# Optimization experiments

Measured on AMD Instinct MI355X. Metric: run time of the kernel, lower is better.

The kernel has to match this reference:

```python
import jax, jax.numpy as jnp
import numpy as np

DIM = 512
DEPTH = 4
E = 2 ** DEPTH          # 16 experts
HID = 4 * DIM           # mult = 4
B, S = 8, 4096


def setup_inputs() -> dict:
    key = jax.random.key(0)
    ks = jax.random.split(key, 7)
    sc_in = 1.0 / np.sqrt(DIM)
    sc_hid = 1.0 / np.sqrt(HID)
    return {
        "x": jax.random.normal(ks[0], (B, S, DIM), jnp.float32),
        "Wr": jax.random.normal(ks[1], (E - 1, DIM), jnp.float32) * sc_in,
        "br": jax.random.normal(ks[2], (E - 1,), jnp.float32) * 0.01,
        "W1": jax.random.normal(ks[3], (E, DIM, HID), jnp.float32) * sc_in,
        "b1": jax.random.normal(ks[4], (E, HID), jnp.float32) * 0.01,
        "W2": jax.random.normal(ks[5], (E, HID, DIM), jnp.float32) * sc_hid,
        "b2": jax.random.normal(ks[6], (E, DIM), jnp.float32) * 0.01,
    }


def _fff_forward(x, Wr, br, W1, b1, W2, b2):
    Bb, Ss, D = x.shape
    E_ = W1.shape[0]
    depth = int(np.log2(E_))
    xf = x.reshape(-1, D)                      # [N, D]
    N = xf.shape[0]

    # Hard binary-tree routing (inference path of the torch module).
    leaf = jnp.zeros((N,), jnp.int32)
    for d in range(depth):
        off = 2 ** d - 1
        cnt = 2 ** d
        # logits for all routers at this tree level: [N, cnt]
        logits = xf @ Wr[off:off + cnt].T + br[off:off + cnt]
        sel = jnp.take_along_axis(logits, leaf[:, None], axis=1)[:, 0]
        leaf = leaf * 2 + (sel > 0).astype(jnp.int32)

    onehot = jax.nn.one_hot(leaf, E_, dtype=xf.dtype)  # [N, E]

    # Dense weighted-sum dispatch: scan over the (small, fixed) expert axis,
    # accumulating masked expert outputs. Peak extra memory is one [N, HID]
    # activation at a time.
    def body(acc, params):
        w1, bb1, w2, bb2, m = params            # m: [N]
        h = jax.nn.gelu(xf @ w1 + bb1, approximate=False)  # exact GELU (torch nn.GELU)
        y = h @ w2 + bb2
        return acc + m[:, None] * y, None

    out, _ = jax.lax.scan(body, jnp.zeros_like(xf), (W1, b1, W2, b2, onehot.T))
    return out.reshape(Bb, Ss, D)


def reference(x, Wr, br, W1, b1, W2, b2):
    return _fff_forward(x, Wr, br, W1, b1, W2, b2)
```

## Files before the change

kernel.cpp:

```cpp
#include <hip/hip_runtime.h>
#include <math.h>

#define NTOK   32768
#define DMODEL 512
#define HIDDEN 2048
#define NEXP   16
#define TM     256
#define MAXT   144
#define PADN   (MAXT * TM)
#define CPAD   16

typedef short bf16x8 __attribute__((ext_vector_type(8)));
typedef float f32x4  __attribute__((ext_vector_type(4)));

__device__ __forceinline__ short f2bf(float f) {
  union { float f; unsigned int u; } v; v.f = f;
  unsigned int r = v.u + 0x7FFFu + ((v.u >> 16) & 1u);
  return (short)(r >> 16);
}

__device__ __forceinline__ void gload_lds16(const void* g, void* l) {
  __builtin_amdgcn_global_load_lds(
      (const __attribute__((address_space(1))) void*)g,
      (__attribute__((address_space(3))) void*)l, 16, 0, 0);
}

__device__ __forceinline__ float gelu_f(float v) {
  const float u = v * (0.7978845608f + 0.0356774081f * v * v);
  const float au = fabsf(u);
  const float z = __expf(-2.0f * au);
  float T = (1.0f - z) / (1.0f + z);
  T = copysignf(T, u);
  return 0.5f * v * (1.0f + T);
}

__global__ void init_kernel(int* counts, int* cursors) {
  counts[threadIdx.x] = 0; cursors[threadIdx.x] = 0;
}

__global__ __launch_bounds__(256) void route_kernel(
    const float* __restrict__ x, const float* __restrict__ Wr,
    const float* __restrict__ br, short* __restrict__ xb,
    int* __restrict__ leafArr) {
  const int w = threadIdx.x >> 6, l = threadIdx.x & 63;
  const int tok = blockIdx.x * 4 + w;
  const float4* xr = (const float4*)(x + (size_t)tok * DMODEL);
  float4 a0 = xr[l * 2], a1 = xr[l * 2 + 1];

  union { bf16x8 v; short s[8]; } u;
  u.s[0] = f2bf(a0.x); u.s[1] = f2bf(a0.y); u.s[2] = f2bf(a0.z); u.s[3] = f2bf(a0.w);
  u.s[4] = f2bf(a1.x); u.s[5] = f2bf(a1.y); u.s[6] = f2bf(a1.z); u.s[7] = f2bf(a1.w);
  *((bf16x8*)(xb + (size_t)tok * DMODEL) + l) = u.v;

  int leaf = 0;
  for (int d = 0; d < 4; ++d) {
    const int node = (1 << d) - 1 + leaf;
    const float4* wr4 = (const float4*)(Wr + (size_t)node * DMODEL);
    float4 b0 = wr4[l * 2], b1v = wr4[l * 2 + 1];
    double s = (double)a0.x * (double)b0.x + (double)a0.y * (double)b0.y +
               (double)a0.z * (double)b0.z + (double)a0.w * (double)b0.w +
               (double)a1.x * (double)b1v.x + (double)a1.y * (double)b1v.y +
               (double)a1.z * (double)b1v.z + (double)a1.w * (double)b1v.w;
    for (int off = 32; off; off >>= 1) s += __shfl_xor(s, off);
    double sel = s + (double)br[node];
    leaf = leaf * 2 + (sel > 0.0 ? 1 : 0);
  }
  if (l == 0) leafArr[tok] = leaf;
}

__global__ __launch_bounds__(256) void count_kernel(
    const int* __restrict__ leafArr, int* __restrict__ counts,
    int* __restrict__ idx) {
  __shared__ int lcnt[NEXP];
  const int tid = threadIdx.x;
  if (tid < NEXP) lcnt[tid] = 0;
  __syncthreads();
  const int tok = blockIdx.x * 256 + tid;
  atomicAdd(&lcnt[leafArr[tok]], 1);
  __syncthreads();
  if (tid < NEXP && lcnt[tid]) atomicAdd(&counts[tid * CPAD], lcnt[tid]);
  for (int i = blockIdx.x * 256 + tid; i < PADN; i += gridDim.x * 256) idx[i] = 0;
}

__global__ void scan_kernel(const int* __restrict__ counts, int* poff, int* ntiles,
                            int* texp, int* tval) {
  if (threadIdx.x == 0) {
    int po = 0, nt = 0;
    for (int e = 0; e < NEXP; ++e) {
      poff[e] = po;
      const int c = counts[e * CPAD];
      const int t = (c + TM - 1) >> 8;
      for (int i = 0; i < t; ++i) {
        texp[nt] = e;
        int v = c - i * TM; if (v > TM) v = TM;
        tval[nt] = v;
        ++nt;
      }
      po += t << 8;
    }
    poff[NEXP] = po;
    *ntiles = nt;
  }
}

__global__ __launch_bounds__(256) void scatter_kernel(
    const int* __restrict__ leafArr, const int* __restrict__ poff,
    int* cursors, int* __restrict__ idx) {
  __shared__ int lcnt[NEXP], lbase[NEXP];
  const int tid = threadIdx.x;
  if (tid < NEXP) lcnt[tid] = 0;
  __syncthreads();
  const int tok = blockIdx.x * 256 + tid;
  const int e = leafArr[tok];
  const int r = atomicAdd(&lcnt[e], 1);
  __syncthreads();
  if (tid < NEXP) lbase[tid] = lcnt[tid] ? atomicAdd(&cursors[tid * CPAD], lcnt[tid]) : 0;
  __syncthreads();
  idx[poff[e] + lbase[e] + r] = tok;
}

__global__ void tconv_kernel(const float* __restrict__ src, short* __restrict__ dst,
                             int R, int C) {
  __shared__ float tile[32][33];
  const int tx = threadIdx.x, ty = threadIdx.y;
  const int c0 = blockIdx.x * 32, r0 = blockIdx.y * 32;
  const size_t eoff = (size_t)blockIdx.z * R * C;
  for (int i = 0; i < 4; ++i)
    tile[ty + i * 8][tx] = src[eoff + (size_t)(r0 + ty + i * 8) * C + c0 + tx];
  __syncthreads();
  for (int i = 0; i < 4; ++i)
    dst[eoff + (size_t)(c0 + ty + i * 8) * R + r0 + tx] = f2bf(tile[tx][ty + i * 8]);
}


#define STA2(pn, ko, J0)                                                       \
  { _Pragma("unroll") for (int j = (J0); j < (J0) + 2; ++j)                    \
      gload_lds16(aSrc[j] + (ko), lds + ((pn) << 14) + j * 4096 + w * 512); }

#define STB4(pn, ko)                                                           \
  { _Pragma("unroll") for (int j = 0; j < 4; ++j)                              \
      gload_lds16(bSrc[j] + (ko), lds + 32768 + ((pn) << 14) + j * 4096 + w * 512); }

#define PHASE(mh, ki, STAGE, POST)                                             \
  {                                                                            \
    bf16x8 af[4];                                                              \
    const int sw_ = ((((ki) << 2) + q) ^ (cc & 7)) << 3;                       \
    _Pragma("unroll")                                                          \
    for (int m2 = 0; m2 < 4; ++m2)                                             \
      af[m2] = *(const bf16x8*)(Ab + (wr + ((mh) * 4 + m2) * 16 + cc) * 64 + sw_); \
    if ((mh) == 0) {                                                           \
      _Pragma("unroll")                                                        \
      for (int ni = 0; ni < 4; ++ni)                                           \
        bfv[ni] = *(const bf16x8*)(Bb + (wc + ni * 16 + cc) * 64 + sw_);       \
    }                                                                          \
    STAGE                                                                      \
    __builtin_amdgcn_s_barrier();                                              \
    __builtin_amdgcn_s_setprio(1);                                             \
    _Pragma("unroll")                                                          \
    for (int m2 = 0; m2 < 4; ++m2) {                                           \
      _Pragma("unroll")                                                        \
      for (int ni = 0; ni < 4; ++ni)                                           \
        acc[(mh) * 4 + m2][ni] = __builtin_amdgcn_mfma_f32_16x16x32_bf16(      \
            af[m2], bfv[ni], acc[(mh) * 4 + m2][ni], 0, 0, 0);                 \
    }                                                                          \
    __builtin_amdgcn_s_setprio(0);                                             \
    POST                                                                       \
    __builtin_amdgcn_s_barrier();                                              \
  }

#define KLOOP(NKT)                                                             \
  STA2(0, 0, 0) STA2(0, 0, 2) STB4(0, 0) STB4(1, 64)                           \
  asm volatile("s_waitcnt vmcnt(4)" ::: "memory");                             \
  __builtin_amdgcn_s_barrier();                                                \
  for (int kt = 0; kt < (NKT); ++kt) {                                         \
    const int cur = kt & 1, pn = cur ^ 1;                                      \
    const short* Ab = lds + (cur << 14);                                       \
    const short* Bb = lds + 32768 + (cur << 14);                               \
    const int ko1 = (kt + 1) << 6, ko2 = (kt + 2) << 6;                        \
    const bool p1ok = kt + 1 < (NKT), p2ok = kt + 2 < (NKT);                   \
    PHASE(0, 0, if (p1ok) STA2(pn, ko1, 0), )                                  \
    PHASE(1, 0, if (p1ok) STA2(pn, ko1, 2), )                                  \
    PHASE(0, 1, , )                                                            \
    PHASE(1, 1, if (p2ok) STB4(cur, ko2),                                      \
          if (p2ok) { asm volatile("s_waitcnt vmcnt(4)" ::: "memory"); }       \
          else      { asm volatile("s_waitcnt vmcnt(0)" ::: "memory"); } )     \
  }

__global__ __launch_bounds__(512, 2) void gemm1_kernel(
    const short* __restrict__ Xb, const short* __restrict__ W1T,
    const float* __restrict__ b1, const int* __restrict__ idx,
    const int* __restrict__ texp, const int* __restrict__ ntiles,
    short* __restrict__ H, int g0) {
  __shared__ short lds[65536];
  const int nb = gridDim.x, bid = blockIdx.x;
  int swz = bid;
  if ((nb & 7) == 0) { const int cpx = nb >> 3; swz = (bid & 7) * cpx + (bid >> 3); }
  const int lt = swz >> 3, cb = swz & 7;
  const int t = g0 + lt;
  if (t >= *ntiles) return;
  const int e = texp[t];
  const int c0 = cb * 256;

  const int tid = threadIdx.x, w = tid >> 6, lane = tid & 63;
  const int q = lane >> 4, cc = lane & 15;
  const int wr = (w >> 2) * 128, wc = (w & 3) * 64;
  const int srow = lane >> 3;
  const int skel = ((lane & 7) ^ srow) * 8;

  const short* aSrc[4]; const short* bSrc[4];
#pragma unroll
  for (int j = 0; j < 4; ++j) {
    const int r = j * 64 + w * 8 + srow;
    const int gt = idx[t * TM + r];
    aSrc[j] = Xb + (size_t)gt * DMODEL + skel;
    bSrc[j] = W1T + ((size_t)e * HIDDEN + c0 + r) * DMODEL + skel;
  }

  f32x4 acc[8][4];
  const f32x4 zero = {0.f, 0.f, 0.f, 0.f};
#pragma unroll
  for (int mi = 0; mi < 8; ++mi)
#pragma unroll
    for (int ni = 0; ni < 4; ++ni) acc[mi][ni] = zero;
  bf16x8 bfv[4];

  KLOOP(DMODEL / 64)

  short* Cs = lds;
#pragma unroll
  for (int ni = 0; ni < 4; ++ni) {
    const int col = wc + ni * 16 + cc;
    const float bv = b1[e * HIDDEN + c0 + col];
#pragma unroll
    for (int mi = 0; mi < 8; ++mi) {
#pragma unroll
      for (int r = 0; r < 4; ++r) {
        const int row = wr + mi * 16 + q * 4 + r;
        const float v = gelu_f(acc[mi][ni][r] + bv);
        Cs[row * 256 + ((((col >> 3) ^ (row & 15)) << 3) | (col & 7))] = f2bf(v);
      }
    }
  }
  __syncthreads();
#pragma unroll
  for (int it = 0; it < 16; ++it) {
    const int lin = tid + it * 512;
    const int row = lin >> 5;
    const int s = lin & 31;
    const bf16x8 vv = *(const bf16x8*)(Cs + row * 256 + s * 8);
    const int ch = s ^ (row & 15);
    *(bf16x8*)(H + ((size_t)lt * TM + row) * HIDDEN + c0 + (ch << 3)) = vv;
  }
}

__global__ __launch_bounds__(512, 2) void gemm2_kernel(
    const short* __restrict__ H, const short* __restrict__ W2T,
    const float* __restrict__ b2, const int* __restrict__ idx,
    const int* __restrict__ texp, const int* __restrict__ tval,
    const int* __restrict__ ntiles, float* __restrict__ out, int g0) {
  __shared__ short lds[65536];
  const int nb = gridDim.x, bid = blockIdx.x;
  int swz = bid;
  if ((nb & 7) == 0) { const int cpx = nb >> 3; swz = (bid & 7) * cpx + (bid >> 3); }
  const int lt = swz >> 1, cb = swz & 1;
  const int t = g0 + lt;
  if (t >= *ntiles) return;
  const int e = texp[t];
  const int c0 = cb * 256;

  const int tid = threadIdx.x, w = tid >> 6, lane = tid & 63;
  const int q = lane >> 4, cc = lane & 15;
  const int wr = (w >> 2) * 128, wc = (w & 3) * 64;
  const int srow = lane >> 3;
  const int skel = ((lane & 7) ^ srow) * 8;

  const short* aSrc[4]; const short* bSrc[4];
#pragma unroll
  for (int j = 0; j < 4; ++j) {
    const int r = j * 64 + w * 8 + srow;
    aSrc[j] = H + ((size_t)lt * TM + r) * HIDDEN + skel;
    bSrc[j] = W2T + ((size_t)e * DMODEL + c0 + r) * HIDDEN + skel;
  }

  f32x4 acc[8][4];
  const f32x4 zero = {0.f, 0.f, 0.f, 0.f};
#pragma unroll
  for (int mi = 0; mi < 8; ++mi)
#pragma unroll
    for (int ni = 0; ni < 4; ++ni) acc[mi][ni] = zero;
  bf16x8 bfv[4];

  KLOOP(HIDDEN / 64)

  const int nv = tval[t];
#pragma unroll
  for (int ni = 0; ni < 4; ++ni) {
    const int col = c0 + wc + ni * 16 + cc;
    const float bv = b2[e * DMODEL + col];
#pragma unroll
    for (int mi = 0; mi < 8; ++mi) {
#pragma unroll
      for (int r = 0; r < 4; ++r) {
        const int row = wr + mi * 16 + q * 4 + r;
        if (row < nv) {
          const int tok = idx[t * TM + row];
          out[(size_t)tok * DMODEL + col] = acc[mi][ni][r] + bv;
        }
      }
    }
  }
}

extern "C" void kernel_launch(void* const* d_in, const int* in_sizes, int n_in,
                              void* d_out, int out_size, void* d_ws, size_t ws_size,
                              hipStream_t stream) {
  (void)in_sizes; (void)n_in; (void)out_size;
  const float* x  = (const float*)d_in[0];
  const float* Wr = (const float*)d_in[1];
  const float* br = (const float*)d_in[2];
  const float* W1 = (const float*)d_in[3];
  const float* b1 = (const float*)d_in[4];
  const float* W2 = (const float*)d_in[5];
  const float* b2 = (const float*)d_in[6];
  float* out = (float*)d_out;
  char* ws = (char*)d_ws;

  int* counts  = (int*)(ws + 0);
  int* cursors = (int*)(ws + 1024);
  int* poff    = (int*)(ws + 2048);
  int* ntiles  = (int*)(ws + 2304);
  int* texp    = (int*)(ws + 4096);
  int* tval    = (int*)(ws + 8192);
  int* leafA   = (int*)(ws + 16384);
  int* idx     = (int*)(ws + 16384 + 131072);

  const size_t MB32 = 33554432ull;
  short* Xb  = (short*)(ws + (1ull << 20));
  short* W1T = (short*)(ws + (1ull << 20) + MB32);
  short* W2T = (short*)(ws + (1ull << 20) + 2 * MB32);
  short* Hb  = (short*)(ws + (1ull << 20) + 3 * MB32);
  const size_t o_h = (1ull << 20) + 3 * MB32;
  const size_t perTile = (size_t)TM * HIDDEN * sizeof(short);

  int TPG = MAXT;
  if (ws_size < o_h + (size_t)MAXT * perTile) {
    size_t avail = ws_size > o_h ? ws_size - o_h : 0;
    TPG = (int)(avail / perTile);
    TPG &= ~3;
    if (TPG < 4) TPG = 4;
  }
  const int ngroups = (MAXT + TPG - 1) / TPG;

  hipLaunchKernelGGL(init_kernel,    dim3(1),          dim3(256),   0, stream, counts, cursors);
  hipLaunchKernelGGL(route_kernel,   dim3(NTOK / 4),   dim3(256),   0, stream, x, Wr, br, Xb, leafA);
  hipLaunchKernelGGL(count_kernel,   dim3(NTOK / 256), dim3(256),   0, stream, leafA, counts, idx);
  hipLaunchKernelGGL(scan_kernel,    dim3(1),          dim3(64),    0, stream, counts, poff, ntiles, texp, tval);
  hipLaunchKernelGGL(scatter_kernel, dim3(NTOK / 256), dim3(256),   0, stream, leafA, poff, cursors, idx);
  hipLaunchKernelGGL(tconv_kernel,   dim3(64, 16, 16), dim3(32, 8), 0, stream, W1, W1T, DMODEL, HIDDEN);
  hipLaunchKernelGGL(tconv_kernel,   dim3(16, 64, 16), dim3(32, 8), 0, stream, W2, W2T, HIDDEN, DMODEL);

  for (int g = 0; g < ngroups; ++g) {
    hipLaunchKernelGGL(gemm1_kernel, dim3(TPG * 8), dim3(512), 0, stream,
                       Xb, W1T, b1, idx, texp, ntiles, Hb, g * TPG);
    hipLaunchKernelGGL(gemm2_kernel, dim3(TPG * 2), dim3(512), 0, stream,
                       Hb, W2T, b2, idx, texp, tval, ntiles, out, g * TPG);
  }
}
```

Baseline: 565.0 us.

## Replace double-buffered pipelined K loop with single-buffer loop for higher occupancy

Drops the two-stage LDS double buffering and phased prefetch in both GEMMs. Each K step now loads a single tile, waits, and computes. LDS per block is halved and the epilogue is split into two halves so it fits, which allows the launch bounds to ask for four blocks per CU. The gain in occupancy comes at the cost of losing load/compute overlap, and the tighter register budget risks spilling the 128-float accumulator.

```diff
diff --git a/kernel.cpp b/kernel.cpp
--- a/kernel.cpp
+++ b/kernel.cpp
@@ -133,65 +133,48 @@
 }
 
 
-#define STA2(pn, ko, J0)                                                       \
-  { _Pragma("unroll") for (int j = (J0); j < (J0) + 2; ++j)                    \
-      gload_lds16(aSrc[j] + (ko), lds + ((pn) << 14) + j * 4096 + w * 512); }
-
-#define STB4(pn, ko)                                                           \
+#define STA1(ko)                                                               \
   { _Pragma("unroll") for (int j = 0; j < 4; ++j)                              \
-      gload_lds16(bSrc[j] + (ko), lds + 32768 + ((pn) << 14) + j * 4096 + w * 512); }
-
-#define PHASE(mh, ki, STAGE, POST)                                             \
-  {                                                                            \
-    bf16x8 af[4];                                                              \
-    const int sw_ = ((((ki) << 2) + q) ^ (cc & 7)) << 3;                       \
-    _Pragma("unroll")                                                          \
-    for (int m2 = 0; m2 < 4; ++m2)                                             \
-      af[m2] = *(const bf16x8*)(Ab + (wr + ((mh) * 4 + m2) * 16 + cc) * 64 + sw_); \
-    if ((mh) == 0) {                                                           \
-      _Pragma("unroll")                                                        \
-      for (int ni = 0; ni < 4; ++ni)                                           \
-        bfv[ni] = *(const bf16x8*)(Bb + (wc + ni * 16 + cc) * 64 + sw_);       \
-    }                                                                          \
-    STAGE                                                                      \
+      gload_lds16(aSrc[j] + (ko), lds + j * 4096 + w * 512); }
+
+#define STB1(ko)                                                               \
+  { _Pragma("unroll") for (int j = 0; j < 4; ++j)                              \
+      gload_lds16(bSrc[j] + (ko), lds + 16384 + j * 4096 + w * 512); }
+
+#define KLOOP_SIMPLE(NKT)                                                      \
+  for (int kt = 0; kt < (NKT); ++kt) {                                         \
+    STA1(kt << 6) STB1(kt << 6)                                                \
+    asm volatile("s_waitcnt vmcnt(0)" ::: "memory");                           \
     __builtin_amdgcn_s_barrier();                                              \
     __builtin_amdgcn_s_setprio(1);                                             \
     _Pragma("unroll")                                                          \
-    for (int m2 = 0; m2 < 4; ++m2) {                                           \
+    for (int ki = 0; ki < 2; ++ki) {                                           \
+      const int sw_ = (((ki << 2) + q) ^ (cc & 7)) << 3;                       \
+      bf16x8 af[8], bfv[4];                                                    \
+      _Pragma("unroll")                                                        \
+      for (int mi = 0; mi < 8; ++mi)                                           \
+        af[mi] = *(const bf16x8*)(lds + (wr + mi * 16 + cc) * 64 + sw_);       \
       _Pragma("unroll")                                                        \
       for (int ni = 0; ni < 4; ++ni)                                           \
-        acc[(mh) * 4 + m2][ni] = __builtin_amdgcn_mfma_f32_16x16x32_bf16(      \
-            af[m2], bfv[ni], acc[(mh) * 4 + m2][ni], 0, 0, 0);                 \
+        bfv[ni] = *(const bf16x8*)(lds + 16384 + (wc + ni * 16 + cc) * 64 + sw_); \
+      _Pragma("unroll")                                                        \
+      for (int mi = 0; mi < 8; ++mi) {                                         \
+        _Pragma("unroll")                                                      \
+        for (int ni = 0; ni < 4; ++ni)                                         \
+          acc[mi][ni] = __builtin_amdgcn_mfma_f32_16x16x32_bf16(               \
+              af[mi], bfv[ni], acc[mi][ni], 0, 0, 0);                          \
+      }                                                                        \
     }                                                                          \
     __builtin_amdgcn_s_setprio(0);                                             \
-    POST                                                                       \
     __builtin_amdgcn_s_barrier();                                              \
   }
 
-#define KLOOP(NKT)                                                             \
-  STA2(0, 0, 0) STA2(0, 0, 2) STB4(0, 0) STB4(1, 64)                           \
-  asm volatile("s_waitcnt vmcnt(4)" ::: "memory");                             \
-  __builtin_amdgcn_s_barrier();                                                \
-  for (int kt = 0; kt < (NKT); ++kt) {                                         \
-    const int cur = kt & 1, pn = cur ^ 1;                                      \
-    const short* Ab = lds + (cur << 14);                                       \
-    const short* Bb = lds + 32768 + (cur << 14);                               \
-    const int ko1 = (kt + 1) << 6, ko2 = (kt + 2) << 6;                        \
-    const bool p1ok = kt + 1 < (NKT), p2ok = kt + 2 < (NKT);                   \
-    PHASE(0, 0, if (p1ok) STA2(pn, ko1, 0), )                                  \
-    PHASE(1, 0, if (p1ok) STA2(pn, ko1, 2), )                                  \
-    PHASE(0, 1, , )                                                            \
-    PHASE(1, 1, if (p2ok) STB4(cur, ko2),                                      \
-          if (p2ok) { asm volatile("s_waitcnt vmcnt(4)" ::: "memory"); }       \
-          else      { asm volatile("s_waitcnt vmcnt(0)" ::: "memory"); } )     \
-  }
-
-__global__ __launch_bounds__(512, 2) void gemm1_kernel(
+__global__ __launch_bounds__(512, 4) void gemm1_kernel(
     const short* __restrict__ Xb, const short* __restrict__ W1T,
     const float* __restrict__ b1, const int* __restrict__ idx,
     const int* __restrict__ texp, const int* __restrict__ ntiles,
     short* __restrict__ H, int g0) {
-  __shared__ short lds[65536];
+  __shared__ short lds[32768];
   const int nb = gridDim.x, bid = blockIdx.x;
   int swz = bid;
   if ((nb & 7) == 0) { const int cpx = nb >> 3; swz = (bid & 7) * cpx + (bid >> 3); }
@@ -222,43 +205,47 @@
   for (int mi = 0; mi < 8; ++mi)
 #pragma unroll
     for (int ni = 0; ni < 4; ++ni) acc[mi][ni] = zero;
-  bf16x8 bfv[4];
-
-  KLOOP(DMODEL / 64)
+
+  KLOOP_SIMPLE(DMODEL / 64)
 
   short* Cs = lds;
-#pragma unroll
-  for (int ni = 0; ni < 4; ++ni) {
-    const int col = wc + ni * 16 + cc;
-    const float bv = b1[e * HIDDEN + c0 + col];
-#pragma unroll
-    for (int mi = 0; mi < 8; ++mi) {
-#pragma unroll
-      for (int r = 0; r < 4; ++r) {
-        const int row = wr + mi * 16 + q * 4 + r;
-        const float v = gelu_f(acc[mi][ni][r] + bv);
-        Cs[row * 256 + ((((col >> 3) ^ (row & 15)) << 3) | (col & 7))] = f2bf(v);
+  for (int h = 0; h < 2; ++h) {
+    if ((w >> 2) == h) {
+#pragma unroll
+      for (int ni = 0; ni < 4; ++ni) {
+        const int col = wc + ni * 16 + cc;
+        const float bv = b1[e * HIDDEN + c0 + col];
+#pragma unroll
+        for (int mi = 0; mi < 8; ++mi) {
+#pragma unroll
+          for (int r = 0; r < 4; ++r) {
+            const int lrow = mi * 16 + q * 4 + r;
+            const float v = gelu_f(acc[mi][ni][r] + bv);
+            Cs[lrow * 256 + ((((col >> 3) ^ (lrow & 15)) << 3) | (col & 7))] = f2bf(v);
+          }
+        }
       }
     }
-  }
-  __syncthreads();
-#pragma unroll
-  for (int it = 0; it < 16; ++it) {
-    const int lin = tid + it * 512;
-    const int row = lin >> 5;
-    const int s = lin & 31;
-    const bf16x8 vv = *(const bf16x8*)(Cs + row * 256 + s * 8);
-    const int ch = s ^ (row & 15);
-    *(bf16x8*)(H + ((size_t)lt * TM + row) * HIDDEN + c0 + (ch << 3)) = vv;
-  }
-}
-
-__global__ __launch_bounds__(512, 2) void gemm2_kernel(
+    __syncthreads();
+#pragma unroll
+    for (int it = 0; it < 8; ++it) {
+      const int lin = tid + it * 512;
+      const int row = lin >> 5;
+      const int s = lin & 31;
+      const bf16x8 vv = *(const bf16x8*)(Cs + row * 256 + s * 8);
+      const int ch = s ^ (row & 15);
+      *(bf16x8*)(H + ((size_t)lt * TM + h * 128 + row) * HIDDEN + c0 + (ch << 3)) = vv;
+    }
+    __syncthreads();
+  }
+}
+
+__global__ __launch_bounds__(512, 4) void gemm2_kernel(
     const short* __restrict__ H, const short* __restrict__ W2T,
     const float* __restrict__ b2, const int* __restrict__ idx,
     const int* __restrict__ texp, const int* __restrict__ tval,
     const int* __restrict__ ntiles, float* __restrict__ out, int g0) {
-  __shared__ short lds[65536];
+  __shared__ short lds[32768];
   const int nb = gridDim.x, bid = blockIdx.x;
   int swz = bid;
   if ((nb & 7) == 0) { const int cpx = nb >> 3; swz = (bid & 7) * cpx + (bid >> 3); }
@@ -288,9 +275,8 @@
   for (int mi = 0; mi < 8; ++mi)
 #pragma unroll
     for (int ni = 0; ni < 4; ++ni) acc[mi][ni] = zero;
-  bf16x8 bfv[4];
-
-  KLOOP(HIDDEN / 64)
+
+  KLOOP_SIMPLE(HIDDEN / 64)
 
   const int nv = tval[t];
 #pragma unroll
```

Result: slower. 1.749 ms (+209.6%).

## Shrink gemm2 output tile to 256x128 with a custom pipelined K loop

Applied to the files above, without the earlier changes.

The second expert GEMM now splits each token tile into four 128-column blocks instead of two 256-column blocks, which doubles the grid and halves the per-wave accumulators and the B-side LDS footprint. It replaces the shared KLOOP macro with a dedicated four-phase loop that stages A and B loads into double-buffered LDS and overlaps them with MFMA using barriers, setprio and explicit vmcnt waits. This targets better occupancy and load balance for the small gemm2 grid, at the cost of reloading the H tile twice as often.

```diff
diff --git a/kernel.cpp b/kernel.cpp
--- a/kernel.cpp
+++ b/kernel.cpp
@@ -253,44 +253,95 @@
   }
 }
 
+#define G2STB2(pn, ko)                                                         \
+  { _Pragma("unroll") for (int j = 0; j < 2; ++j)                              \
+      gload_lds16(bSrc[j] + (ko), lds + 32768 + (pn) * 8192 + j * 4096 + w * 512); }
+
+#define G2PHASE(mh, ki, STAGE, POST)                                           \
+  {                                                                            \
+    bf16x8 af[2];                                                              \
+    const int sw_ = ((((ki) << 2) + q) ^ (cc & 7)) << 3;                       \
+    _Pragma("unroll")                                                          \
+    for (int m2 = 0; m2 < 2; ++m2)                                             \
+      af[m2] = *(const bf16x8*)(Ab + (wr + ((mh) * 2 + m2) * 16 + cc) * 64 + sw_); \
+    if ((mh) == 0) {                                                           \
+      _Pragma("unroll")                                                        \
+      for (int ni = 0; ni < 4; ++ni)                                           \
+        bfv[ni] = *(const bf16x8*)(Bb + (wc + ni * 16 + cc) * 64 + sw_);       \
+    }                                                                          \
+    STAGE                                                                      \
+    __builtin_amdgcn_s_barrier();                                              \
+    __builtin_amdgcn_s_setprio(1);                                             \
+    _Pragma("unroll")                                                          \
+    for (int m2 = 0; m2 < 2; ++m2) {                                           \
+      _Pragma("unroll")                                                        \
+      for (int ni = 0; ni < 4; ++ni)                                           \
+        acc[(mh) * 2 + m2][ni] = __builtin_amdgcn_mfma_f32_16x16x32_bf16(      \
+            af[m2], bfv[ni], acc[(mh) * 2 + m2][ni], 0, 0, 0);                 \
+    }                                                                          \
+    __builtin_amdgcn_s_setprio(0);                                             \
+    POST                                                                       \
+    __builtin_amdgcn_s_barrier();                                              \
+  }
+
 __global__ __launch_bounds__(512, 2) void gemm2_kernel(
     const short* __restrict__ H, const short* __restrict__ W2T,
     const float* __restrict__ b2, const int* __restrict__ idx,
     const int* __restrict__ texp, const int* __restrict__ tval,
     const int* __restrict__ ntiles, float* __restrict__ out, int g0) {
-  __shared__ short lds[65536];
+  __shared__ short lds[49152];
   const int nb = gridDim.x, bid = blockIdx.x;
   int swz = bid;
   if ((nb & 7) == 0) { const int cpx = nb >> 3; swz = (bid & 7) * cpx + (bid >> 3); }
-  const int lt = swz >> 1, cb = swz & 1;
+  const int lt = swz >> 2, cb = swz & 3;
   const int t = g0 + lt;
   if (t >= *ntiles) return;
   const int e = texp[t];
-  const int c0 = cb * 256;
+  const int c0 = cb * 128;
 
   const int tid = threadIdx.x, w = tid >> 6, lane = tid & 63;
   const int q = lane >> 4, cc = lane & 15;
-  const int wr = (w >> 2) * 128, wc = (w & 3) * 64;
+  const int wr = (w >> 1) * 64, wc = (w & 1) * 64;
   const int srow = lane >> 3;
   const int skel = ((lane & 7) ^ srow) * 8;
 
-  const short* aSrc[4]; const short* bSrc[4];
+  const short* aSrc[4]; const short* bSrc[2];
 #pragma unroll
   for (int j = 0; j < 4; ++j) {
     const int r = j * 64 + w * 8 + srow;
     aSrc[j] = H + ((size_t)lt * TM + r) * HIDDEN + skel;
+  }
+#pragma unroll
+  for (int j = 0; j < 2; ++j) {
+    const int r = j * 64 + w * 8 + srow;
     bSrc[j] = W2T + ((size_t)e * DMODEL + c0 + r) * HIDDEN + skel;
   }
 
-  f32x4 acc[8][4];
+  f32x4 acc[4][4];
   const f32x4 zero = {0.f, 0.f, 0.f, 0.f};
 #pragma unroll
-  for (int mi = 0; mi < 8; ++mi)
+  for (int mi = 0; mi < 4; ++mi)
 #pragma unroll
     for (int ni = 0; ni < 4; ++ni) acc[mi][ni] = zero;
   bf16x8 bfv[4];
 
-  KLOOP(HIDDEN / 64)
+  STA2(0, 0, 0) STA2(0, 0, 2) G2STB2(0, 0) G2STB2(1, 64)
+  asm volatile("s_waitcnt vmcnt(2)" ::: "memory");
+  __builtin_amdgcn_s_barrier();
+
+  for (int kt = 0; kt < HIDDEN / 64; ++kt) {
+    const int cur = kt & 1, pn = cur ^ 1;
+    const short* Ab = lds + (cur << 14);
+    const short* Bb = lds + 32768 + cur * 8192;
+    const int ko1 = (kt + 1) << 6, ko2 = (kt + 2) << 6;
+    const bool p1ok = kt + 1 < HIDDEN / 64, p2ok = kt + 2 < HIDDEN / 64;
+    G2PHASE(0, 0, if (p1ok) STA2(pn, ko1, 0), )
+    G2PHASE(1, 0, if (p1ok) STA2(pn, ko1, 2), )
+    G2PHASE(0, 1, , )
+    G2PHASE(1, 1, if (p2ok) G2STB2(cur, ko2),
+            if (p2ok) { asm volatile("s_waitcnt vmcnt(2)" ::: "memory"); }
+            else      { asm volatile("s_waitcnt vmcnt(0)" ::: "memory"); } )
+  }
 
   const int nv = tval[t];
 #pragma unroll
@@ -298,7 +349,7 @@
     const int col = c0 + wc + ni * 16 + cc;
     const float bv = b2[e * DMODEL + col];
 #pragma unroll
-    for (int mi = 0; mi < 8; ++mi) {
+    for (int mi = 0; mi < 4; ++mi) {
 #pragma unroll
       for (int r = 0; r < 4; ++r) {
         const int row = wr + mi * 16 + q * 4 + r;
@@ -362,7 +413,7 @@
   for (int g = 0; g < ngroups; ++g) {
     hipLaunchKernelGGL(gemm1_kernel, dim3(TPG * 8), dim3(512), 0, stream,
                        Xb, W1T, b1, idx, texp, ntiles, Hb, g * TPG);
-    hipLaunchKernelGGL(gemm2_kernel, dim3(TPG * 2), dim3(512), 0, stream,
+    hipLaunchKernelGGL(gemm2_kernel, dim3(TPG * 4), dim3(512), 0, stream,
                        Hb, W2T, b2, idx, texp, tval, ntiles, out, g * TPG);
   }
 }
```

New measurement: 555.5 us. Within noise of the previous version (-1.7%).
